# Optimization experiments

Hardware: AMD Instinct MI355X
Metric: run time of the kernel (lower is better)

Reference implementation:

```python
import jax, jax.numpy as jnp
import numpy as np

B, S, D, H = 4, 2048, 1024, 16
DK = D // H

def setup_inputs() -> dict:
    key = jax.random.key(0)
    ks = jax.random.split(key, 7)
    f = lambda k, shape: jax.random.normal(k, shape, dtype=jnp.float32)
    return {
        "query": f(ks[0], (B, S, D)),
        "key":   f(ks[1], (B, S, D)),
        "value": f(ks[2], (B, S, D)),
        "w_q": f(ks[3], (D, D)) * (D ** -0.5),
        "w_k": f(ks[4], (D, D)) * (D ** -0.5),
        "w_v": f(ks[5], (D, D)) * (D ** -0.5),
        "w_o": f(ks[6], (D, D)) * (D ** -0.5),
    }

def reference(query, key, value, w_q, w_k, w_v, w_o):
    # Linear layers: y = x @ W^T (torch nn.Linear convention), bias=False
    def split_heads(x):  # [B,S,D] -> [B,H,S,DK]
        return x.reshape(B, S, H, DK).transpose(0, 2, 1, 3)
    Q = split_heads(query @ w_q.T)
    K = split_heads(key @ w_k.T)
    V = split_heads(value @ w_v.T)
    scale = jnp.float32(1.0 / np.sqrt(DK))
    scores = jnp.einsum('bhqd,bhkd->bhqk', Q, K) * scale  # [B,H,Sq,Sk]
    attn = jax.nn.softmax(scores, axis=-1)
    out = jnp.einsum('bhqk,bhkd->bhqd', attn, V)  # [B,H,Sq,DK]
    out = out.transpose(0, 2, 1, 3).reshape(B, S, D)
    return out @ w_o.T
```

## Files before the change

kernel.cpp:

```cpp
#include <hip/hip_runtime.h>
#include <stdint.h>

#define NB 4
#define NS 2048
#define ND 1024
#define NH 16
#define NDK 64
#define NM (NB*NS)

typedef __attribute__((ext_vector_type(8))) short short8;
typedef __attribute__((ext_vector_type(8))) unsigned short ushort8v;
typedef __attribute__((ext_vector_type(4))) float f32x4;
typedef __attribute__((ext_vector_type(16))) float f32x16;

__device__ __forceinline__ unsigned short f2bf(float f) {
  union { float f; uint32_t u; } v; v.f = f;
  uint32_t u = v.u;
  return (unsigned short)((u + 0x7FFFu + ((u >> 16) & 1u)) >> 16);
}

__device__ __forceinline__ void gload16(const void* g, void* l) {
  __builtin_amdgcn_global_load_lds(
      (const __attribute__((address_space(1))) void*)g,
      (__attribute__((address_space(3))) void*)l, 16, 0, 0);
}

__device__ __forceinline__ int xcd_swz(int flat, int nwg) {
  return (flat & 7) * (nwg >> 3) + (flat >> 3);
}

__global__ void convert_all(
    const float* __restrict__ x0, const float* __restrict__ x1, const float* __restrict__ x2,
    const float* __restrict__ w0, const float* __restrict__ w1,
    const float* __restrict__ w2, const float* __restrict__ w3,
    unsigned short* __restrict__ ox0, unsigned short* __restrict__ ox1, unsigned short* __restrict__ ox2,
    unsigned short* __restrict__ ow0, unsigned short* __restrict__ ow1,
    unsigned short* __restrict__ ow2, unsigned short* __restrict__ ow3)
{
  const float* src;
  unsigned short* dst;
  size_t i;
  if (blockIdx.y < 3) {
    src = blockIdx.y == 0 ? x0 : (blockIdx.y == 1 ? x1 : x2);
    dst = blockIdx.y == 0 ? ox0 : (blockIdx.y == 1 ? ox1 : ox2);
    i = ((size_t)blockIdx.x * 256 + threadIdx.x) * 8;
  } else {
    if (blockIdx.x >= 2048) return;
    size_t e = ((size_t)blockIdx.x * 256 + threadIdx.x) * 8;
    int which = (int)(e >> 20);
    size_t off = e & ((1u << 20) - 1);
    const float* ws[4] = {w0, w1, w2, w3};
    unsigned short* wd[4] = {ow0, ow1, ow2, ow3};
    src = ws[which]; dst = wd[which]; i = off;
  }
  f32x4 a = *(const f32x4*)(src + i);
  f32x4 b = *(const f32x4*)(src + i + 4);
  ushort8v h;
  h[0]=f2bf(a.x); h[1]=f2bf(a.y); h[2]=f2bf(a.z); h[3]=f2bf(a.w);
  h[4]=f2bf(b.x); h[5]=f2bf(b.y); h[6]=f2bf(b.z); h[7]=f2bf(b.w);
  *(ushort8v*)(dst + i) = h;
}

#define GPHASE(MH, NH, LA, LB)                                                 \
  {                                                                            \
    if (LA) {                                                                  \
      _Pragma("unroll") for (int mm = 0; mm < 4; ++mm)                         \
        _Pragma("unroll") for (int kk = 0; kk < 2; ++kk)                       \
          af[mm][kk] = *(const short8*)(Ab + (MH)*8192 + mm*2048 + rowb + aoff[kk]); \
    }                                                                          \
    if (LB) {                                                                  \
      _Pragma("unroll") for (int nn = 0; nn < NN; ++nn)                        \
        _Pragma("unroll") for (int kk = 0; kk < 2; ++kk)                       \
          bf[nn][kk] = *(const short8*)(Bb + (NH)*(NN*2048) + nn*2048 + rowb + aoff[kk]); \
    }                                                                          \
    __builtin_amdgcn_s_setprio(1);                                             \
    _Pragma("unroll") for (int mm = 0; mm < 4; ++mm)                           \
      _Pragma("unroll") for (int nn = 0; nn < NN; ++nn)                        \
        _Pragma("unroll") for (int kk = 0; kk < 2; ++kk)                       \
          acc[(MH)*4+mm][(NH)*NN+nn] = __builtin_amdgcn_mfma_f32_16x16x32_bf16( \
              af[mm][kk], bf[nn][kk], acc[(MH)*4+mm][(NH)*NN+nn], 0, 0, 0);    \
    __builtin_amdgcn_s_setprio(0);                                             \
  }

template<int OUT, int PRESCALE, int BN>
__device__ __forceinline__ void gemm256_core(
    const unsigned short* __restrict__ A,
    const unsigned short* __restrict__ Bt,
    void* __restrict__ Cout,
    unsigned short* lds, int m0, int n0)
{
  const int K = ND, N = ND;
  const int NN = BN / 128;
  const int NBL = BN / 64;
  const int ASZ = 16384, BSZ = BN * 64, SZ = ASZ + BSZ;
  const int tid = threadIdx.x;
  const int lane = tid & 63, wid = tid >> 6;
  const int l15 = lane & 15, lg = lane >> 4;
  const int wr = wid >> 2, wc = wid & 3;
  const float QSC = 0.125f * 1.44269504088896f;

  const unsigned short* Asrc[4];
  const unsigned short* Bsrc[NBL];
#pragma unroll
  for (int l = 0; l < 4; ++l) {
    int cidx = l*512 + tid;
    int r = cidx >> 3;
    int cs = ((cidx & 7) ^ (r & 7)) * 8;
    Asrc[l] = A + (size_t)(m0 + r)*K + cs;
  }
#pragma unroll
  for (int l = 0; l < NBL; ++l) {
    int cidx = l*512 + tid;
    int r = cidx >> 3;
    int cs = ((cidx & 7) ^ (r & 7)) * 8;
    Bsrc[l] = Bt + (size_t)(n0 + r)*K + cs;
  }

  const int rowb = l15 * 128;
  int aoff[2];
  aoff[0] = ((lg)     ^ (l15 & 7)) * 16;
  aoff[1] = ((4 + lg) ^ (l15 & 7)) * 16;

  f32x4 acc[8][2*NN] = {};
  short8 af[4][2], bf[NN][2];

#pragma unroll
  for (int l = 0; l < 4; ++l) gload16(Asrc[l], lds + l*4096 + tid*8);
#pragma unroll
  for (int l = 0; l < NBL; ++l) gload16(Bsrc[l], lds + ASZ + l*4096 + tid*8);
  asm volatile("s_waitcnt vmcnt(0)" ::: "memory");
  __builtin_amdgcn_s_barrier();

  const int NT = K / 64;
  for (int t = 0; t < NT; ++t) {
    const int cur = t & 1;
    if (t + 1 < NT) {
      unsigned short* dst = lds + (cur^1)*SZ;
#pragma unroll
      for (int l = 0; l < 4; ++l) gload16(Asrc[l] + (t+1)*64, dst + l*4096 + tid*8);
#pragma unroll
      for (int l = 0; l < NBL; ++l) gload16(Bsrc[l] + (t+1)*64, dst + ASZ + l*4096 + tid*8);
    }
    const char* Ab = (const char*)(lds + cur*SZ) + wr*16384;
    const char* Bb = (const char*)(lds + cur*SZ + ASZ) + wc*(BN*32);

    GPHASE(0, 0, 1, 1)
    GPHASE(0, 1, 0, 1)
    GPHASE(1, 1, 1, 0)
    GPHASE(1, 0, 0, 1)

    asm volatile("s_waitcnt vmcnt(0)" ::: "memory");
    __builtin_amdgcn_s_barrier();
  }

#pragma unroll
  for (int m = 0; m < 8; ++m)
#pragma unroll
    for (int n = 0; n < 2*NN; ++n)
#pragma unroll
      for (int i = 0; i < 4; ++i) {
        int row = m0 + wr*128 + m*16 + lg*4 + i;
        int col = n0 + wc*(BN/4) + n*16 + l15;
        float val = PRESCALE ? acc[m][n][i] * QSC : acc[m][n][i];
        if (OUT == 0)
          ((float*)Cout)[(size_t)row * N + col] = val;
        else if (OUT == 1)
          ((unsigned short*)Cout)[(size_t)row * N + col] = f2bf(val);
        else
          ((unsigned short*)Cout)[((size_t)((row >> 11)*1024 + col))*NS + (row & (NS-1))]
              = f2bf(val);
      }
}

__global__ __launch_bounds__(512, 1) void gemm_qkv(
    const unsigned short* __restrict__ Xq, const unsigned short* __restrict__ Wq, unsigned short* Qb,
    const unsigned short* __restrict__ Xk, const unsigned short* __restrict__ Wk, unsigned short* Kb,
    const unsigned short* __restrict__ Xv, const unsigned short* __restrict__ Wv, unsigned short* VbT)
{
  __shared__ unsigned short lds[65536];
  int flat = (blockIdx.z * 32 + blockIdx.y) * 4 + blockIdx.x;
  int swz = xcd_swz(flat, 384);
  int z = swz >> 7, rem = swz & 127;
  int m0 = (rem >> 2) * 256, n0 = (rem & 3) * 256;
  if (z == 0)      gemm256_core<1,1,256>(Xq, Wq, Qb,  lds, m0, n0);
  else if (z == 1) gemm256_core<1,0,256>(Xk, Wk, Kb,  lds, m0, n0);
  else             gemm256_core<2,0,256>(Xv, Wv, VbT, lds, m0, n0);
}

__global__ __launch_bounds__(512, 1) void gemm_o(
    const unsigned short* __restrict__ A, const unsigned short* __restrict__ Bt, float* C)
{
  __shared__ unsigned short lds[49152];
  int flat = blockIdx.y * 8 + blockIdx.x;
  int swz = xcd_swz(flat, 256);
  gemm256_core<0,0,128>(A, Bt, C, lds, (swz >> 3) * 256, (swz & 7) * 128);
}

__global__ __launch_bounds__(256, 2) void flash_attn(
    const unsigned short* __restrict__ Qb,
    const unsigned short* __restrict__ Kb,
    const unsigned short* __restrict__ VT,
    unsigned short* __restrict__ O)
{
  __shared__ unsigned short Kt[2][64*64];
  __shared__ unsigned short Vt[2][64*64];
  const int tid = threadIdx.x, lane = tid & 63, wid = tid >> 6;
  const int l31 = lane & 31, hi = lane >> 5;
  int flat = blockIdx.y * 8 + blockIdx.x;
  int swz = xcd_swz(flat, 512);
  const int bh = swz >> 3, b = bh >> 4, h = bh & 15;
  const int q0 = (swz & 7) * 256 + wid * 64;

  const unsigned short* Kp[2]; const unsigned short* Vp[2]; int dofs[2];
#pragma unroll
  for (int p = 0; p < 2; ++p) {
    int slot = tid + p*256;
    int g = slot >> 6, r = slot & 63;
    Kp[p] = Kb + ((size_t)(b*NS + r))*ND + h*64 + g*8;
    Vp[p] = VT + ((size_t)(bh*64 + r))*NS + g*8;
    dofs[p] = slot * 8;
  }

  short8 qf[2][4];
#pragma unroll
  for (int qs = 0; qs < 2; ++qs)
#pragma unroll
    for (int ks = 0; ks < 4; ++ks)
      qf[qs][ks] = *(const short8*)(Qb + (size_t)(b*NS + q0 + qs*32 + l31)*ND + h*64 + ks*16 + hi*8);

  f32x16 oacc[2][2] = {};
  float lsum[2] = {0.f, 0.f};

#pragma unroll
  for (int p = 0; p < 2; ++p) {
    gload16(Kp[p], &Kt[0][dofs[p]]);
    gload16(Vp[p], &Vt[0][dofs[p]]);
  }
  __syncthreads();

  for (int t = 0; t < NS/64; ++t) {
    const int cur = t & 1;
    if (t + 1 < NS/64) {
#pragma unroll
      for (int p = 0; p < 2; ++p) {
        gload16(Kp[p] + (size_t)(t+1)*64*ND, &Kt[cur^1][dofs[p]]);
        gload16(Vp[p] + (t+1)*64,            &Vt[cur^1][dofs[p]]);
      }
    }
    const char* Kc = (const char*)Kt[cur];
    const char* Vc = (const char*)Vt[cur];

    short8 pa[2][2][2];
    float rs[2] = {0.f, 0.f};

#pragma unroll
    for (int n = 0; n < 2; ++n) {
      f32x16 st[2] = {};
      const int r = n*32 + l31;
      __builtin_amdgcn_s_setprio(1);
#pragma unroll
      for (int ks = 0; ks < 4; ++ks) {
        short8 kf = *(const short8*)(Kc + (((2*ks + hi) << 10) + r*16));
        st[0] = __builtin_amdgcn_mfma_f32_32x32x16_bf16(kf, qf[0][ks], st[0], 0, 0, 0);
        st[1] = __builtin_amdgcn_mfma_f32_32x32x16_bf16(kf, qf[1][ks], st[1], 0, 0, 0);
      }
      __builtin_amdgcn_s_setprio(0);
#pragma unroll
      for (int qs = 0; qs < 2; ++qs) {
        float lrs = 0.f;
#pragma unroll
        for (int e = 0; e < 16; ++e) {
          float p = __builtin_amdgcn_exp2f(st[qs][e]);
          st[qs][e] = p;
          lrs += p;
        }
        rs[qs] += lrs;
        uint32_t w[4][2];
#pragma unroll
        for (int e = 0; e < 4; ++e) {
          asm("v_cvt_pk_bf16_f32 %0, %1, %2"
              : "=v"(w[e][0]) : "v"(st[qs][4*e+0]), "v"(st[qs][4*e+1]));
          asm("v_cvt_pk_bf16_f32 %0, %1, %2"
              : "=v"(w[e][1]) : "v"(st[qs][4*e+2]), "v"(st[qs][4*e+3]));
        }
#pragma unroll
        for (int ksl = 0; ksl < 2; ++ksl) {
          uint32_t a0 = w[2*ksl][0], b0 = w[2*ksl+1][0];
          uint32_t a1 = w[2*ksl][1], b1 = w[2*ksl+1][1];
          asm("v_permlane32_swap_b32 %0, %1" : "+v"(a0), "+v"(b0));
          asm("v_permlane32_swap_b32 %0, %1" : "+v"(a1), "+v"(b1));
          union { uint32_t u[4]; short8 s; } f;
          f.u[0] = a0; f.u[1] = a1; f.u[2] = b0; f.u[3] = b1;
          pa[qs][n][ksl] = f.s;
        }
      }
    }
#pragma unroll
    for (int qs = 0; qs < 2; ++qs) {
      rs[qs] += __shfl_xor(rs[qs], 32);
      lsum[qs] += rs[qs];
    }

    __builtin_amdgcn_s_setprio(1);
#pragma unroll
    for (int d = 0; d < 2; ++d) {
      const int dr = d*32 + l31;
#pragma unroll
      for (int n = 0; n < 2; ++n)
#pragma unroll
        for (int ksl = 0; ksl < 2; ++ksl) {
          const int g = n*4 + ksl*2 + hi;
          short8 vf = *(const short8*)(Vc + ((g << 10) + dr*16));
          oacc[0][d] = __builtin_amdgcn_mfma_f32_32x32x16_bf16(pa[0][n][ksl], vf, oacc[0][d], 0, 0, 0);
          oacc[1][d] = __builtin_amdgcn_mfma_f32_32x32x16_bf16(pa[1][n][ksl], vf, oacc[1][d], 0, 0, 0);
        }
    }
    __builtin_amdgcn_s_setprio(0);
    __syncthreads();
  }

#pragma unroll
  for (int qs = 0; qs < 2; ++qs) {
    float linv[16];
#pragma unroll
    for (int r = 0; r < 16; ++r)
      linv[r] = 1.0f / __shfl(lsum[qs], (r & 3) + 8*(r >> 2) + 4*hi);
#pragma unroll
    for (int d = 0; d < 2; ++d)
#pragma unroll
      for (int r = 0; r < 16; ++r) {
        int qrow = q0 + qs*32 + (r & 3) + 8*(r >> 2) + 4*hi;
        O[(size_t)(b*NS + qrow)*ND + h*64 + d*32 + l31] = f2bf(oacc[qs][d][r] * linv[r]);
      }
  }
}

extern "C" void kernel_launch(void* const* d_in, const int* in_sizes, int n_in,
                              void* d_out, int out_size, void* d_ws, size_t ws_size,
                              hipStream_t stream) {
  const float* q  = (const float*)d_in[0];
  const float* k  = (const float*)d_in[1];
  const float* v  = (const float*)d_in[2];
  const float* wq = (const float*)d_in[3];
  const float* wk = (const float*)d_in[4];
  const float* wv = (const float*)d_in[5];
  const float* wo = (const float*)d_in[6];

  unsigned short* Wq = (unsigned short*)d_ws;
  unsigned short* Wk = Wq + (size_t)ND*ND;
  unsigned short* Wv = Wk + (size_t)ND*ND;
  unsigned short* Wo = Wv + (size_t)ND*ND;
  unsigned short* Xq = Wo + (size_t)ND*ND;
  unsigned short* Xk = Xq + (size_t)NM*ND;
  unsigned short* Xv = Xk + (size_t)NM*ND;
  unsigned short* Qb = Xv + (size_t)NM*ND;
  unsigned short* Kb = Qb + (size_t)NM*ND;
  unsigned short* VbT = (unsigned short*)d_out;
  unsigned short* Ob  = Xq;

  convert_all<<<dim3(NM*ND/(256*8), 4), 256, 0, stream>>>(
      q, k, v, wq, wk, wv, wo, Xq, Xk, Xv, Wq, Wk, Wv, Wo);

  gemm_qkv<<<dim3(4, 32, 3), 512, 0, stream>>>(Xq, Wq, Qb, Xk, Wk, Kb, Xv, Wv, VbT);

  flash_attn<<<dim3(8, 64), 256, 0, stream>>>(Qb, Kb, VbT, Ob);

  gemm_o<<<dim3(8, 32), 512, 0, stream>>>(Ob, Wo, (float*)d_out);
}
```

Measured before the change: 203.4 us.

## Switch GEMM core to BK=32 triple-buffered LDS pipeline with prefetch depth two

The shared GEMM core used by the QKV and output projections now walks K in 32-wide tiles instead of 64-wide, with three LDS buffers and loads issued two tiles ahead. It waits with partial vmcnt so one tile's loads stay in flight across the barrier. A new XOR swizzle matches the 64-byte rows. The aim is to hide global-to-LDS latency better and shrink LDS per stage. The cost is twice as many barriers and loop iterations, and less MFMA work per sync.

```diff
diff --git a/kernel.cpp b/kernel.cpp
--- a/kernel.cpp
+++ b/kernel.cpp
@@ -61,102 +61,111 @@
   *(ushort8v*)(dst + i) = h;
 }
 
-#define GPHASE(MH, NH, LA, LB)                                                 \
-  {                                                                            \
-    if (LA) {                                                                  \
-      _Pragma("unroll") for (int mm = 0; mm < 4; ++mm)                         \
-        _Pragma("unroll") for (int kk = 0; kk < 2; ++kk)                       \
-          af[mm][kk] = *(const short8*)(Ab + (MH)*8192 + mm*2048 + rowb + aoff[kk]); \
-    }                                                                          \
-    if (LB) {                                                                  \
-      _Pragma("unroll") for (int nn = 0; nn < NN; ++nn)                        \
-        _Pragma("unroll") for (int kk = 0; kk < 2; ++kk)                       \
-          bf[nn][kk] = *(const short8*)(Bb + (NH)*(NN*2048) + nn*2048 + rowb + aoff[kk]); \
-    }                                                                          \
-    __builtin_amdgcn_s_setprio(1);                                             \
-    _Pragma("unroll") for (int mm = 0; mm < 4; ++mm)                           \
-      _Pragma("unroll") for (int nn = 0; nn < NN; ++nn)                        \
-        _Pragma("unroll") for (int kk = 0; kk < 2; ++kk)                       \
-          acc[(MH)*4+mm][(NH)*NN+nn] = __builtin_amdgcn_mfma_f32_16x16x32_bf16( \
-              af[mm][kk], bf[nn][kk], acc[(MH)*4+mm][(NH)*NN+nn], 0, 0, 0);    \
-    __builtin_amdgcn_s_setprio(0);                                             \
-  }
-
 template<int OUT, int PRESCALE, int BN>
-__device__ __forceinline__ void gemm256_core(
+__device__ __forceinline__ void gemm_bk32_core(
     const unsigned short* __restrict__ A,
     const unsigned short* __restrict__ Bt,
     void* __restrict__ Cout,
     unsigned short* lds, int m0, int n0)
 {
   const int K = ND, N = ND;
-  const int NN = BN / 128;
-  const int NBL = BN / 64;
-  const int ASZ = 16384, BSZ = BN * 64, SZ = ASZ + BSZ;
+  const int NBF = BN / 64;
+  const int NBL = BN / 128;
+  const int NL  = 2 + NBL;
+  const int ASZ = 8192, BSZ = BN*32, SZ = ASZ + BSZ;
+  const int NT = K / 32;
   const int tid = threadIdx.x;
   const int lane = tid & 63, wid = tid >> 6;
   const int l15 = lane & 15, lg = lane >> 4;
   const int wr = wid >> 2, wc = wid & 3;
   const float QSC = 0.125f * 1.44269504088896f;
 
-  const unsigned short* Asrc[4];
-  const unsigned short* Bsrc[NBL];
-#pragma unroll
-  for (int l = 0; l < 4; ++l) {
+  const unsigned short* Asrc[2];
+  const unsigned short* Bsrc[2];
+  int dofA[2], dofB[2];
+#pragma unroll
+  for (int l = 0; l < 2; ++l) {
     int cidx = l*512 + tid;
-    int r = cidx >> 3;
-    int cs = ((cidx & 7) ^ (r & 7)) * 8;
-    Asrc[l] = A + (size_t)(m0 + r)*K + cs;
+    int r = cidx >> 2;
+    int ch = (cidx & 3) ^ ((r >> 1) & 3);
+    Asrc[l] = A + (size_t)(m0 + r)*K + ch*8;
+    dofA[l] = cidx * 8;
   }
 #pragma unroll
   for (int l = 0; l < NBL; ++l) {
     int cidx = l*512 + tid;
-    int r = cidx >> 3;
-    int cs = ((cidx & 7) ^ (r & 7)) * 8;
-    Bsrc[l] = Bt + (size_t)(n0 + r)*K + cs;
-  }
-
-  const int rowb = l15 * 128;
-  int aoff[2];
-  aoff[0] = ((lg)     ^ (l15 & 7)) * 16;
-  aoff[1] = ((4 + lg) ^ (l15 & 7)) * 16;
-
-  f32x4 acc[8][2*NN] = {};
-  short8 af[4][2], bf[NN][2];
-
-#pragma unroll
-  for (int l = 0; l < 4; ++l) gload16(Asrc[l], lds + l*4096 + tid*8);
-#pragma unroll
-  for (int l = 0; l < NBL; ++l) gload16(Bsrc[l], lds + ASZ + l*4096 + tid*8);
-  asm volatile("s_waitcnt vmcnt(0)" ::: "memory");
+    int r = cidx >> 2;
+    int ch = (cidx & 3) ^ ((r >> 1) & 3);
+    Bsrc[l] = Bt + (size_t)(n0 + r)*K + ch*8;
+    dofB[l] = cidx * 8;
+  }
+
+  f32x4 acc[8][NBF] = {};
+
+#define STAGE32(t, buf)                                                        \
+  {                                                                            \
+    unsigned short* d_ = lds + (buf)*SZ;                                       \
+    _Pragma("unroll") for (int l = 0; l < 2; ++l)                              \
+      gload16(Asrc[l] + (t)*32, d_ + dofA[l]);                                 \
+    _Pragma("unroll") for (int l = 0; l < NBL; ++l)                            \
+      gload16(Bsrc[l] + (t)*32, d_ + ASZ + dofB[l]);                           \
+  }
+
+  STAGE32(0, 0)
+  STAGE32(1, 1)
+  if (NBL == 2) asm volatile("s_waitcnt vmcnt(4)" ::: "memory");
+  else          asm volatile("s_waitcnt vmcnt(3)" ::: "memory");
   __builtin_amdgcn_s_barrier();
 
-  const int NT = K / 64;
+  int b0 = 0;
   for (int t = 0; t < NT; ++t) {
-    const int cur = t & 1;
-    if (t + 1 < NT) {
-      unsigned short* dst = lds + (cur^1)*SZ;
-#pragma unroll
-      for (int l = 0; l < 4; ++l) gload16(Asrc[l] + (t+1)*64, dst + l*4096 + tid*8);
-#pragma unroll
-      for (int l = 0; l < NBL; ++l) gload16(Bsrc[l] + (t+1)*64, dst + ASZ + l*4096 + tid*8);
-    }
-    const char* Ab = (const char*)(lds + cur*SZ) + wr*16384;
-    const char* Bb = (const char*)(lds + cur*SZ + ASZ) + wc*(BN*32);
-
-    GPHASE(0, 0, 1, 1)
-    GPHASE(0, 1, 0, 1)
-    GPHASE(1, 1, 1, 0)
-    GPHASE(1, 0, 0, 1)
-
-    asm volatile("s_waitcnt vmcnt(0)" ::: "memory");
-    __builtin_amdgcn_s_barrier();
-  }
+    if (t + 2 < NT) {
+      int nb = b0 + 2; if (nb >= 3) nb -= 3;
+      STAGE32(t + 2, nb)
+    }
+    const unsigned short* Abase = lds + b0*SZ;
+    const unsigned short* Bbase = lds + b0*SZ + ASZ;
+
+    short8 bfr[NBF];
+#pragma unroll
+    for (int nn = 0; nn < NBF; ++nn) {
+      int row = wc*(BN/4) + nn*16 + l15;
+      bfr[nn] = *(const short8*)(Bbase + row*32 + (lg ^ ((row >> 1) & 3))*8);
+    }
+#pragma unroll
+    for (int mh = 0; mh < 2; ++mh) {
+      short8 af[4];
+#pragma unroll
+      for (int mm = 0; mm < 4; ++mm) {
+        int row = wr*128 + mh*64 + mm*16 + l15;
+        af[mm] = *(const short8*)(Abase + row*32 + (lg ^ ((row >> 1) & 3))*8);
+      }
+      __builtin_amdgcn_s_setprio(1);
+#pragma unroll
+      for (int mm = 0; mm < 4; ++mm)
+#pragma unroll
+        for (int nn = 0; nn < NBF; ++nn)
+          acc[mh*4+mm][nn] = __builtin_amdgcn_mfma_f32_16x16x32_bf16(
+              af[mm], bfr[nn], acc[mh*4+mm][nn], 0, 0, 0);
+      __builtin_amdgcn_s_setprio(0);
+    }
+
+    if (t + 2 < NT) {
+      if (NBL == 2) asm volatile("s_waitcnt vmcnt(4)" ::: "memory");
+      else          asm volatile("s_waitcnt vmcnt(3)" ::: "memory");
+      __builtin_amdgcn_s_barrier();
+    } else if (t + 1 < NT) {
+      asm volatile("s_waitcnt vmcnt(0)" ::: "memory");
+      __builtin_amdgcn_s_barrier();
+    }
+    b0 = (b0 + 1 == 3) ? 0 : b0 + 1;
+  }
+#undef STAGE32
 
 #pragma unroll
   for (int m = 0; m < 8; ++m)
 #pragma unroll
-    for (int n = 0; n < 2*NN; ++n)
+    for (int n = 0; n < NBF; ++n)
 #pragma unroll
       for (int i = 0; i < 4; ++i) {
         int row = m0 + wr*128 + m*16 + lg*4 + i;
@@ -177,23 +186,23 @@
     const unsigned short* __restrict__ Xk, const unsigned short* __restrict__ Wk, unsigned short* Kb,
     const unsigned short* __restrict__ Xv, const unsigned short* __restrict__ Wv, unsigned short* VbT)
 {
-  __shared__ unsigned short lds[65536];
+  __shared__ unsigned short lds[3*16384];
   int flat = (blockIdx.z * 32 + blockIdx.y) * 4 + blockIdx.x;
   int swz = xcd_swz(flat, 384);
   int z = swz >> 7, rem = swz & 127;
   int m0 = (rem >> 2) * 256, n0 = (rem & 3) * 256;
-  if (z == 0)      gemm256_core<1,1,256>(Xq, Wq, Qb,  lds, m0, n0);
-  else if (z == 1) gemm256_core<1,0,256>(Xk, Wk, Kb,  lds, m0, n0);
-  else             gemm256_core<2,0,256>(Xv, Wv, VbT, lds, m0, n0);
+  if (z == 0)      gemm_bk32_core<1,1,256>(Xq, Wq, Qb,  lds, m0, n0);
+  else if (z == 1) gemm_bk32_core<1,0,256>(Xk, Wk, Kb,  lds, m0, n0);
+  else             gemm_bk32_core<2,0,256>(Xv, Wv, VbT, lds, m0, n0);
 }
 
 __global__ __launch_bounds__(512, 1) void gemm_o(
     const unsigned short* __restrict__ A, const unsigned short* __restrict__ Bt, float* C)
 {
-  __shared__ unsigned short lds[49152];
+  __shared__ unsigned short lds[3*12288];
   int flat = blockIdx.y * 8 + blockIdx.x;
   int swz = xcd_swz(flat, 256);
-  gemm256_core<0,0,128>(A, Bt, C, lds, (swz >> 3) * 256, (swz & 7) * 128);
+  gemm_bk32_core<0,0,128>(A, Bt, C, lds, (swz >> 3) * 256, (swz & 7) * 128);
 }
 
 __global__ __launch_bounds__(256, 2) void flash_attn(
```

After: 200.4 us. About the same (-1.5%).
